# Kernel tuning notes

Measured on AMD Instinct MI355X. Metric: run time of the kernel, lower is better.

## Reference

```python
import jax, jax.numpy as jnp
import numpy as np

D_MODEL = 1024
NUM_HEADS = 16

def setup_inputs() -> dict:
    key = jax.random.key(0)
    ks = jax.random.split(key, 9)
    d = D_MODEL
    s = 0.02
    return {
        "x": jax.random.normal(ks[0], (2, 2048, d), dtype=jnp.float32),
        "wq": jax.random.normal(ks[1], (d, d), dtype=jnp.float32) * s,
        "bq": jax.random.normal(ks[2], (d,), dtype=jnp.float32) * s,
        "wk": jax.random.normal(ks[3], (d, d), dtype=jnp.float32) * s,
        "bk": jax.random.normal(ks[4], (d,), dtype=jnp.float32) * s,
        "wv": jax.random.normal(ks[5], (d, d), dtype=jnp.float32) * s,
        "bv": jax.random.normal(ks[6], (d,), dtype=jnp.float32) * s,
        "wo": jax.random.normal(ks[7], (d, d), dtype=jnp.float32) * s,
        "bo": jax.random.normal(ks[8], (d,), dtype=jnp.float32) * s,
    }

def reference(x, wq, bq, wk, bk, wv, bv, wo, bo) -> jnp.ndarray:
    b, s, d = x.shape
    h = NUM_HEADS
    dk = d // h
    # projections (torch Linear: x @ W^T + b)
    q = x @ wq.T + bq
    k = x @ wk.T + bk
    v = x @ wv.T + bv
    # split heads -> [b, h, s, dk]
    q = q.reshape(b, s, h, dk).transpose(0, 2, 1, 3)
    k = k.reshape(b, s, h, dk).transpose(0, 2, 1, 3)
    v = v.reshape(b, s, h, dk).transpose(0, 2, 1, 3)
    scale = jnp.sqrt(jnp.asarray(dk, dtype=x.dtype))
    scores = jnp.einsum('bhqd,bhkd->bhqk', q, k) / scale
    causal = jnp.tril(jnp.ones((s, s), dtype=bool))  # [s, s]
    scores = jnp.where(causal[None, None], scores, jnp.asarray(-jnp.inf, dtype=x.dtype))
    attn = jax.nn.softmax(scores, axis=-1)
    out = jnp.einsum('bhqk,bhkd->bhqd', attn, v)
    out = out.transpose(0, 2, 1, 3).reshape(b, s, d)
    return out @ wo.T + bo
```

## Files before the change

### kernel.cpp

```cpp
#include <hip/hip_runtime.h>

#define D_MODEL 1024
#define NHEAD   16
#define DK      64
#define BATCH   2
#define SEQ     2048
#define M_TOT   (BATCH*SEQ)

typedef unsigned short u16;
typedef unsigned int   u32;
typedef __attribute__((ext_vector_type(8))) __bf16 bf16x8;
typedef __attribute__((ext_vector_type(8))) u16   u16x8;
typedef __attribute__((ext_vector_type(4))) u16   u16x4;
typedef __attribute__((ext_vector_type(4))) float f32x4;

typedef const __attribute__((address_space(1))) u32* gas_ptr;
typedef __attribute__((address_space(3))) u32*       las_ptr;

__device__ __forceinline__ void gload16(const u16* g, u16* l) {
  __builtin_amdgcn_global_load_lds((gas_ptr)g, (las_ptr)l, 16, 0, 0);
}

__device__ __forceinline__ u16 bfc(float f) {
  union { __bf16 h; u16 u; } v; v.h = (__bf16)f; return v.u;
}

__global__ void cvt_all(const float* __restrict__ x,
                        const float* __restrict__ wq, const float* __restrict__ wk,
                        const float* __restrict__ wv, const float* __restrict__ wo,
                        u16* __restrict__ xbf, u16* __restrict__ wbf) {
  const int y = blockIdx.y;
  const float* src;
  u16* dst;
  int n8;
  if (y == 0)      { src = x;  dst = xbf;                n8 = M_TOT * D_MODEL / 8; }
  else if (y == 1) { src = wq; dst = wbf;                n8 = 1024 * 1024 / 8; }
  else if (y == 2) { src = wk; dst = wbf + 1 * 1048576;  n8 = 1024 * 1024 / 8; }
  else if (y == 3) { src = wv; dst = wbf + 2 * 1048576;  n8 = 1024 * 1024 / 8; }
  else             { src = wo; dst = wbf + 3 * 1048576;  n8 = 1024 * 1024 / 8; }
  for (int i = blockIdx.x * blockDim.x + threadIdx.x; i < n8; i += gridDim.x * blockDim.x) {
    const float4* s = (const float4*)src + (size_t)i * 2;
    float4 a = s[0], b = s[1];
    u16x8 o;
    o[0]=bfc(a.x); o[1]=bfc(a.y); o[2]=bfc(a.z); o[3]=bfc(a.w);
    o[4]=bfc(b.x); o[5]=bfc(b.y); o[6]=bfc(b.z); o[7]=bfc(b.w);
    *((u16x8*)dst + i) = o;
  }
}

#define QSCALE 0.18033688011112042f

__global__ __launch_bounds__(256) void qkv_gemm(
    const u16* __restrict__ xbf, const u16* __restrict__ wbf,
    const float* __restrict__ bq, const float* __restrict__ bk, const float* __restrict__ bv,
    u16* __restrict__ qws, u16* __restrict__ kws, u16* __restrict__ vtws)
{
  __shared__ u16 la[2 * 128 * 32];
  __shared__ u16 lb[2 * 64 * 32];
  const int z     = blockIdx.z;
  const int nbase = blockIdx.x * 64;
  const int mbase = blockIdx.y * 128;
  const u16*  A    = xbf;
  const u16*  Bm   = wbf + (size_t)z * 1024 * 1024;
  const float* bias = (z == 0) ? bq : (z == 1) ? bk : bv;

  const int tid  = threadIdx.x;
  const int lane = tid & 63;
  const int wid  = tid >> 6;
  const int wr   = (wid >> 1) * 64, wc = (wid & 1) * 32;
  const int lr   = lane & 15, lg = lane >> 4;
  const int srow = tid >> 2;
  const int sc   = tid & 3;
  const int sdst = srow * 32 + sc * 8;
  const int ssrc = (sc ^ ((srow >> 1) & 3)) * 8;
  const int csw  = (lg ^ ((lr >> 1) & 3)) * 8;

  f32x4 acc[4][2];
  #pragma unroll
  for (int i = 0; i < 4; ++i) { acc[i][0] = (f32x4){0,0,0,0}; acc[i][1] = (f32x4){0,0,0,0}; }

  {
    gload16(&A [(size_t)(mbase + srow)      * 1024 + ssrc], &la[sdst]);
    gload16(&A [(size_t)(mbase + srow + 64) * 1024 + ssrc], &la[64*32 + sdst]);
    gload16(&Bm[(size_t)(nbase + srow)      * 1024 + ssrc], &lb[sdst]);
  }
  __syncthreads();
  int cur = 0;
  for (int k0 = 0; k0 < 1024; k0 += 32) {
    if (k0 + 32 < 1024) {
      const int nb = cur ^ 1;
      gload16(&A [(size_t)(mbase + srow)      * 1024 + k0 + 32 + ssrc], &la[nb*4096 + sdst]);
      gload16(&A [(size_t)(mbase + srow + 64) * 1024 + k0 + 32 + ssrc], &la[nb*4096 + 64*32 + sdst]);
      gload16(&Bm[(size_t)(nbase + srow)      * 1024 + k0 + 32 + ssrc], &lb[nb*2048 + sdst]);
    }
    bf16x8 af[4], bfr[2];
    #pragma unroll
    for (int i = 0; i < 4; ++i)
      af[i] = *(const bf16x8*)&la[cur*4096 + (wr + i*16 + lr)*32 + csw];
    #pragma unroll
    for (int j = 0; j < 2; ++j)
      bfr[j] = *(const bf16x8*)&lb[cur*2048 + (wc + j*16 + lr)*32 + csw];
    #pragma unroll
    for (int i = 0; i < 4; ++i)
      #pragma unroll
      for (int j = 0; j < 2; ++j)
        acc[i][j] = __builtin_amdgcn_mfma_f32_16x16x32_bf16(af[i], bfr[j], acc[i][j], 0, 0, 0);
    __syncthreads();
    cur ^= 1;
  }

  #pragma unroll
  for (int i = 0; i < 4; ++i) {
    #pragma unroll
    for (int j = 0; j < 2; ++j) {
      int gn = nbase + wc + j*16 + lr;
      float bs = bias[gn];
      int h = gn >> 6, d = gn & 63;
      int gm0 = mbase + wr + i*16 + lg*4;
      int bb = gm0 >> 11, s0 = gm0 & 2047;
      if (z == 2) {
        u16x4 vk;
        #pragma unroll
        for (int r = 0; r < 4; ++r) vk[r] = bfc(acc[i][j][r] + bs);
        *(u16x4*)&vtws[(((size_t)(bb*NHEAD + h)) * DK + d) * SEQ + s0] = vk;
      } else {
        #pragma unroll
        for (int r = 0; r < 4; ++r) {
          float v = acc[i][j][r] + bs;
          if (z == 0) qws[(((size_t)(bb*NHEAD + h)) * SEQ + s0 + r) * DK + d] = bfc(v * QSCALE);
          else        kws[(((size_t)(bb*NHEAD + h)) * SEQ + s0 + r) * DK + d] = bfc(v);
        }
      }
    }
  }
}

__global__ __launch_bounds__(256) void out_gemm(
    const u16* __restrict__ ows, const u16* __restrict__ wobf,
    const float* __restrict__ bo, float* __restrict__ out)
{
  __shared__ u16 la[2 * 64 * 64];
  __shared__ u16 lb[2 * 64 * 64];
  const int nbase = blockIdx.x * 64;
  const int mbase = blockIdx.y * 64;
  const int tid  = threadIdx.x;
  const int lane = tid & 63;
  const int wid  = tid >> 6;
  const int wr   = (wid >> 1) * 32, wc = (wid & 1) * 32;
  const int lr   = lane & 15, lg = lane >> 4;
  const int srow = tid >> 3;
  const int sc   = tid & 7;
  const int sdst = srow * 64 + sc * 8;
  const int ssrc = (sc ^ (srow & 7)) * 8;
  const int lsw  = lr & 7;

  f32x4 acc[2][2];
  acc[0][0] = (f32x4){0,0,0,0}; acc[0][1] = (f32x4){0,0,0,0};
  acc[1][0] = (f32x4){0,0,0,0}; acc[1][1] = (f32x4){0,0,0,0};

  {
    gload16(&ows [(size_t)(mbase + srow)      * 1024 + ssrc], &la[sdst]);
    gload16(&ows [(size_t)(mbase + srow + 32) * 1024 + ssrc], &la[32*64 + sdst]);
    gload16(&wobf[(size_t)(nbase + srow)      * 1024 + ssrc], &lb[sdst]);
    gload16(&wobf[(size_t)(nbase + srow + 32) * 1024 + ssrc], &lb[32*64 + sdst]);
  }
  __syncthreads();
  int cur = 0;
  for (int k0 = 0; k0 < 1024; k0 += 64) {
    if (k0 + 64 < 1024) {
      const int nb = cur ^ 1;
      gload16(&ows [(size_t)(mbase + srow)      * 1024 + k0 + 64 + ssrc], &la[nb*4096 + sdst]);
      gload16(&ows [(size_t)(mbase + srow + 32) * 1024 + k0 + 64 + ssrc], &la[nb*4096 + 32*64 + sdst]);
      gload16(&wobf[(size_t)(nbase + srow)      * 1024 + k0 + 64 + ssrc], &lb[nb*4096 + sdst]);
      gload16(&wobf[(size_t)(nbase + srow + 32) * 1024 + k0 + 64 + ssrc], &lb[nb*4096 + 32*64 + sdst]);
    }
    bf16x8 af[2][2], bfr[2][2];
    #pragma unroll
    for (int kk = 0; kk < 2; ++kk) {
      #pragma unroll
      for (int i = 0; i < 2; ++i)
        af[i][kk] = *(const bf16x8*)&la[cur*4096 + (wr + i*16 + lr)*64 + (((kk*4 + lg) ^ lsw) * 8)];
      #pragma unroll
      for (int j = 0; j < 2; ++j)
        bfr[j][kk] = *(const bf16x8*)&lb[cur*4096 + (wc + j*16 + lr)*64 + (((kk*4 + lg) ^ lsw) * 8)];
    }
    #pragma unroll
    for (int kk = 0; kk < 2; ++kk)
      #pragma unroll
      for (int i = 0; i < 2; ++i)
        #pragma unroll
        for (int j = 0; j < 2; ++j)
          acc[i][j] = __builtin_amdgcn_mfma_f32_16x16x32_bf16(af[i][kk], bfr[j][kk], acc[i][j], 0, 0, 0);
    __syncthreads();
    cur ^= 1;
  }

  #pragma unroll
  for (int i = 0; i < 2; ++i) {
    #pragma unroll
    for (int j = 0; j < 2; ++j) {
      int gn = nbase + wc + j*16 + lr;
      float bs = bo[gn];
      #pragma unroll
      for (int r = 0; r < 4; ++r) {
        int gm = mbase + wr + i*16 + lg*4 + r;
        out[(size_t)gm * 1024 + gn] = acc[i][j][r] + bs;
      }
    }
  }
}

__global__ __launch_bounds__(256) void attn_kernel(
    const u16* __restrict__ qws, const u16* __restrict__ kws,
    const u16* __restrict__ vtws, u16* __restrict__ ows)
{
  __shared__ u16 kbuf[2 * 64 * 64];
  __shared__ u16 vbuf[2 * 64 * 64];
  __shared__ u16 pbuf[4 * 16 * 64];
  const int flat = blockIdx.x;
  const int r    = flat & 7;
  const int g    = flat >> 3;
  const int bh_l = g >> 5;
  const int qp   = g & 31;
  const int qt   = (bh_l & 1) ? qp : (31 - qp);
  const int bh   = r * 4 + bh_l;
  const int b = bh >> 4, h = bh & 15;
  const int tid = threadIdx.x, wid = tid >> 6, lane = tid & 63;
  const int lr = lane & 15, lg = lane >> 4;
  const u16* Q  = qws  + (size_t)(b * NHEAD + h) * SEQ * DK;
  const u16* K  = kws  + (size_t)(b * NHEAD + h) * SEQ * DK;
  const u16* Vt = vtws + (size_t)(b * NHEAD + h) * DK * SEQ;

  const int sr  = tid >> 3;
  const int sc8 = (tid & 7) * 8;
  const int c0s = ((tid & 7) ^ (sr & 7)) * 8;
  const int c1s = ((tid & 7) ^ ((sr + 32) & 7)) * 8;

  #define STAGE(u, bi) do { \
    const int kb_ = (u) * 64; \
    const int off_ = (bi) * 4096; \
    gload16(&K[(size_t)(kb_ + sr) * DK + c0s],        &kbuf[off_ + sr * 64 + sc8]); \
    gload16(&K[(size_t)(kb_ + sr + 32) * DK + c1s],   &kbuf[off_ + (sr + 32) * 64 + sc8]); \
    gload16(&Vt[(size_t)sr * SEQ + kb_ + c0s],        &vbuf[off_ + sr * 64 + sc8]); \
    gload16(&Vt[(size_t)(sr + 32) * SEQ + kb_ + c1s], &vbuf[off_ + (sr + 32) * 64 + sc8]); \
  } while (0)
  #define CH(m) ((((m)*4 + lg) ^ (lr & 7)) * 8)

  const int qbase  = qt * 64 + wid * 16;
  const int q_glob = qbase + lr;

  bf16x8 qf0 = *(const bf16x8*)&Q[(size_t)q_glob * DK + lg * 8];
  bf16x8 qf1 = *(const bf16x8*)&Q[(size_t)q_glob * DK + 32 + lg * 8];

  f32x4 oacc[4];
  #pragma unroll
  for (int t = 0; t < 4; ++t) oacc[t] = (f32x4){0.f, 0.f, 0.f, 0.f};
  float l_run = 0.f;

  STAGE(0, 0);
  __syncthreads();

  int cur = 0;
  for (int t = 0; t <= qt; ++t) {
    if (t < qt) STAGE(t + 1, cur ^ 1);

    const int diag = (t == qt);
    const int nsub = diag ? (wid + 1) : 4;
    const int cb = cur * 4096;

    f32x4 sacc[4];
    __builtin_amdgcn_s_setprio(1);
    #pragma unroll
    for (int ts = 0; ts < 4; ++ts) {
      if (ts >= nsub) continue;
      bf16x8 kf0 = *(const bf16x8*)&kbuf[cb + (ts*16 + lr) * 64 + CH(0)];
      bf16x8 kf1 = *(const bf16x8*)&kbuf[cb + (ts*16 + lr) * 64 + CH(1)];
      f32x4 s0 = (f32x4){0.f, 0.f, 0.f, 0.f};
      s0 = __builtin_amdgcn_mfma_f32_16x16x32_bf16(kf0, qf0, s0, 0, 0, 0);
      s0 = __builtin_amdgcn_mfma_f32_16x16x32_bf16(kf1, qf1, s0, 0, 0, 0);
      sacc[ts] = s0;
    }
    __builtin_amdgcn_s_setprio(0);
    if (diag) {
      const int ts = wid;
      #pragma unroll
      for (int r2 = 0; r2 < 4; ++r2)
        if (lg * 4 + r2 > lr) sacc[ts][r2] = -1e30f;
    }
    #pragma unroll
    for (int ts = 0; ts < 4; ++ts) {
      if (ts >= nsub) continue;
      #pragma unroll
      for (int r2 = 0; r2 < 4; ++r2) {
        float p = __builtin_amdgcn_exp2f(sacc[ts][r2]);
        sacc[ts][r2] = p;
        l_run += p;
      }
    }

    #pragma unroll
    for (int ts = 0; ts < 4; ++ts) {
      u16x4 pk;
      if (ts < nsub) {
        pk[0] = bfc(sacc[ts][0]); pk[1] = bfc(sacc[ts][1]);
        pk[2] = bfc(sacc[ts][2]); pk[3] = bfc(sacc[ts][3]);
      } else {
        pk[0] = 0; pk[1] = 0; pk[2] = 0; pk[3] = 0;
      }
      const int pc = (((ts*2 + (lg >> 1)) ^ (lr & 7)) * 8) + (lg & 1) * 4;
      *(u16x4*)&pbuf[wid * 1024 + lr * 64 + pc] = pk;
    }
    asm volatile("s_waitcnt lgkmcnt(0)" ::: "memory");
    __builtin_amdgcn_sched_barrier(0);
    bf16x8 pf0 = *(const bf16x8*)&pbuf[wid * 1024 + lr * 64 + CH(0)];
    bf16x8 pf1 = *(const bf16x8*)&pbuf[wid * 1024 + lr * 64 + CH(1)];

    __builtin_amdgcn_s_setprio(1);
    #pragma unroll
    for (int td = 0; td < 4; ++td) {
      bf16x8 vf0 = *(const bf16x8*)&vbuf[cb + (td*16 + lr) * 64 + CH(0)];
      bf16x8 vf1 = *(const bf16x8*)&vbuf[cb + (td*16 + lr) * 64 + CH(1)];
      oacc[td] = __builtin_amdgcn_mfma_f32_16x16x32_bf16(vf0, pf0, oacc[td], 0, 0, 0);
      oacc[td] = __builtin_amdgcn_mfma_f32_16x16x32_bf16(vf1, pf1, oacc[td], 0, 0, 0);
    }
    __builtin_amdgcn_s_setprio(0);
    __syncthreads();
    cur ^= 1;
  }

  float l_tot = l_run;
  l_tot += __shfl_xor(l_tot, 16);
  l_tot += __shfl_xor(l_tot, 32);
  const float inv = 1.0f / l_tot;
  #pragma unroll
  for (int td = 0; td < 4; ++td) {
    u16x4 ok;
    #pragma unroll
    for (int r2 = 0; r2 < 4; ++r2) ok[r2] = bfc(oacc[td][r2] * inv);
    *(u16x4*)&ows[((size_t)(b * SEQ + q_glob)) * D_MODEL + h * DK + td*16 + lg*4] = ok;
  }
  #undef CH
  #undef STAGE
}

extern "C" void kernel_launch(void* const* d_in, const int* in_sizes, int n_in,
                              void* d_out, int out_size, void* d_ws, size_t ws_size,
                              hipStream_t stream) {
  const float* x  = (const float*)d_in[0];
  const float* wq = (const float*)d_in[1];
  const float* bq = (const float*)d_in[2];
  const float* wk = (const float*)d_in[3];
  const float* bk = (const float*)d_in[4];
  const float* wv = (const float*)d_in[5];
  const float* bv = (const float*)d_in[6];
  const float* wo = (const float*)d_in[7];
  const float* bo = (const float*)d_in[8];
  float* out = (float*)d_out;

  char* ws = (char*)d_ws;
  u16* qws  = (u16*)(ws + (size_t) 0 * (1 << 20));
  u16* kws  = (u16*)(ws + (size_t) 8 * (1 << 20));
  u16* vtws = (u16*)(ws + (size_t)16 * (1 << 20));
  u16* ows  = (u16*)(ws + (size_t)24 * (1 << 20));
  u16* xbf  = (u16*)(ws + (size_t)32 * (1 << 20));
  u16* wbf  = (u16*)(ws + (size_t)40 * (1 << 20));

  cvt_all<<<dim3(512, 5), 256, 0, stream>>>(x, wq, wk, wv, wo, xbf, wbf);

  qkv_gemm<<<dim3(1024 / 64, M_TOT / 128, 3), 256, 0, stream>>>(
      xbf, wbf, bq, bk, bv, qws, kws, vtws);

  attn_kernel<<<dim3(1024, 1, 1), 256, 0, stream>>>(qws, kws, vtws, ows);

  out_gemm<<<dim3(1024 / 64, M_TOT / 64), 256, 0, stream>>>(
      ows, wbf + (size_t)3 * 1024 * 1024, bo, out);
}
```

Measured before the change: 111.6 us.

## Prefetch two stages ahead with explicit vmcnt waits in GEMMs and attention

Replaces the simple double-buffer loops in the QKV projection, output projection and attention kernels with a two-deep prefetch. Two tiles are issued up front, each iteration waits with a partial s_waitcnt vmcnt so only the oldest tile's loads must have landed, and raw s_barrier calls fenced by sched_barrier replace __syncthreads. This keeps more global-to-LDS loads in flight so memory latency overlaps with MFMA work. The hand-counted vmcnt values must match the number of loads issued per stage, or the code reads stale data.

```diff
diff --git a/kernel.cpp b/kernel.cpp
--- a/kernel.cpp
+++ b/kernel.cpp
@@ -24,6 +24,12 @@
 __device__ __forceinline__ u16 bfc(float f) {
   union { __bf16 h; u16 u; } v; v.h = (__bf16)f; return v.u;
 }
+
+#define BAR() do { \
+  __builtin_amdgcn_sched_barrier(0); \
+  __builtin_amdgcn_s_barrier(); \
+  __builtin_amdgcn_sched_barrier(0); \
+} while (0)
 
 __global__ void cvt_all(const float* __restrict__ x,
                         const float* __restrict__ wq, const float* __restrict__ wk,
@@ -79,35 +85,36 @@
   #pragma unroll
   for (int i = 0; i < 4; ++i) { acc[i][0] = (f32x4){0,0,0,0}; acc[i][1] = (f32x4){0,0,0,0}; }
 
-  {
-    gload16(&A [(size_t)(mbase + srow)      * 1024 + ssrc], &la[sdst]);
-    gload16(&A [(size_t)(mbase + srow + 64) * 1024 + ssrc], &la[64*32 + sdst]);
-    gload16(&Bm[(size_t)(nbase + srow)      * 1024 + ssrc], &lb[sdst]);
-  }
-  __syncthreads();
-  int cur = 0;
-  for (int k0 = 0; k0 < 1024; k0 += 32) {
-    if (k0 + 32 < 1024) {
-      const int nb = cur ^ 1;
-      gload16(&A [(size_t)(mbase + srow)      * 1024 + k0 + 32 + ssrc], &la[nb*4096 + sdst]);
-      gload16(&A [(size_t)(mbase + srow + 64) * 1024 + k0 + 32 + ssrc], &la[nb*4096 + 64*32 + sdst]);
-      gload16(&Bm[(size_t)(nbase + srow)      * 1024 + k0 + 32 + ssrc], &lb[nb*2048 + sdst]);
-    }
+  #define STAGEQ(u, bi) do { \
+    const int k0_ = (u) * 32; \
+    gload16(&A [(size_t)(mbase + srow)      * 1024 + k0_ + ssrc], &la[(bi)*4096 + sdst]); \
+    gload16(&A [(size_t)(mbase + srow + 64) * 1024 + k0_ + ssrc], &la[(bi)*4096 + 64*32 + sdst]); \
+    gload16(&Bm[(size_t)(nbase + srow)      * 1024 + k0_ + ssrc], &lb[(bi)*2048 + sdst]); \
+  } while (0)
+
+  STAGEQ(0, 0);
+  STAGEQ(1, 1);
+  for (int t = 0; t < 32; ++t) {
+    if (t < 31) asm volatile("s_waitcnt vmcnt(3)" ::: "memory");
+    else        asm volatile("s_waitcnt vmcnt(0)" ::: "memory");
+    BAR();
+    const int cb = (t & 1) * 4096, cbb = (t & 1) * 2048;
     bf16x8 af[4], bfr[2];
     #pragma unroll
     for (int i = 0; i < 4; ++i)
-      af[i] = *(const bf16x8*)&la[cur*4096 + (wr + i*16 + lr)*32 + csw];
+      af[i] = *(const bf16x8*)&la[cb + (wr + i*16 + lr)*32 + csw];
     #pragma unroll
     for (int j = 0; j < 2; ++j)
-      bfr[j] = *(const bf16x8*)&lb[cur*2048 + (wc + j*16 + lr)*32 + csw];
+      bfr[j] = *(const bf16x8*)&lb[cbb + (wc + j*16 + lr)*32 + csw];
     #pragma unroll
     for (int i = 0; i < 4; ++i)
       #pragma unroll
       for (int j = 0; j < 2; ++j)
         acc[i][j] = __builtin_amdgcn_mfma_f32_16x16x32_bf16(af[i], bfr[j], acc[i][j], 0, 0, 0);
-    __syncthreads();
-    cur ^= 1;
-  }
+    BAR();
+    if (t + 2 < 32) STAGEQ(t + 2, t & 1);
+  }
+  #undef STAGEQ
 
   #pragma unroll
   for (int i = 0; i < 4; ++i) {
@@ -158,31 +165,30 @@
   acc[0][0] = (f32x4){0,0,0,0}; acc[0][1] = (f32x4){0,0,0,0};
   acc[1][0] = (f32x4){0,0,0,0}; acc[1][1] = (f32x4){0,0,0,0};
 
-  {
-    gload16(&ows [(size_t)(mbase + srow)      * 1024 + ssrc], &la[sdst]);
-    gload16(&ows [(size_t)(mbase + srow + 32) * 1024 + ssrc], &la[32*64 + sdst]);
-    gload16(&wobf[(size_t)(nbase + srow)      * 1024 + ssrc], &lb[sdst]);
-    gload16(&wobf[(size_t)(nbase + srow + 32) * 1024 + ssrc], &lb[32*64 + sdst]);
-  }
-  __syncthreads();
-  int cur = 0;
-  for (int k0 = 0; k0 < 1024; k0 += 64) {
-    if (k0 + 64 < 1024) {
-      const int nb = cur ^ 1;
-      gload16(&ows [(size_t)(mbase + srow)      * 1024 + k0 + 64 + ssrc], &la[nb*4096 + sdst]);
-      gload16(&ows [(size_t)(mbase + srow + 32) * 1024 + k0 + 64 + ssrc], &la[nb*4096 + 32*64 + sdst]);
-      gload16(&wobf[(size_t)(nbase + srow)      * 1024 + k0 + 64 + ssrc], &lb[nb*4096 + sdst]);
-      gload16(&wobf[(size_t)(nbase + srow + 32) * 1024 + k0 + 64 + ssrc], &lb[nb*4096 + 32*64 + sdst]);
-    }
+  #define STAGEO(u, bi) do { \
+    const int k0_ = (u) * 64; \
+    gload16(&ows [(size_t)(mbase + srow)      * 1024 + k0_ + ssrc], &la[(bi)*4096 + sdst]); \
+    gload16(&ows [(size_t)(mbase + srow + 32) * 1024 + k0_ + ssrc], &la[(bi)*4096 + 32*64 + sdst]); \
+    gload16(&wobf[(size_t)(nbase + srow)      * 1024 + k0_ + ssrc], &lb[(bi)*4096 + sdst]); \
+    gload16(&wobf[(size_t)(nbase + srow + 32) * 1024 + k0_ + ssrc], &lb[(bi)*4096 + 32*64 + sdst]); \
+  } while (0)
+
+  STAGEO(0, 0);
+  STAGEO(1, 1);
+  for (int t = 0; t < 16; ++t) {
+    if (t < 15) asm volatile("s_waitcnt vmcnt(4)" ::: "memory");
+    else        asm volatile("s_waitcnt vmcnt(0)" ::: "memory");
+    BAR();
+    const int cb = (t & 1) * 4096;
     bf16x8 af[2][2], bfr[2][2];
     #pragma unroll
     for (int kk = 0; kk < 2; ++kk) {
       #pragma unroll
       for (int i = 0; i < 2; ++i)
-        af[i][kk] = *(const bf16x8*)&la[cur*4096 + (wr + i*16 + lr)*64 + (((kk*4 + lg) ^ lsw) * 8)];
+        af[i][kk] = *(const bf16x8*)&la[cb + (wr + i*16 + lr)*64 + (((kk*4 + lg) ^ lsw) * 8)];
       #pragma unroll
       for (int j = 0; j < 2; ++j)
-        bfr[j][kk] = *(const bf16x8*)&lb[cur*4096 + (wc + j*16 + lr)*64 + (((kk*4 + lg) ^ lsw) * 8)];
+        bfr[j][kk] = *(const bf16x8*)&lb[cb + (wc + j*16 + lr)*64 + (((kk*4 + lg) ^ lsw) * 8)];
     }
     #pragma unroll
     for (int kk = 0; kk < 2; ++kk)
@@ -191,9 +197,10 @@
         #pragma unroll
         for (int j = 0; j < 2; ++j)
           acc[i][j] = __builtin_amdgcn_mfma_f32_16x16x32_bf16(af[i][kk], bfr[j][kk], acc[i][j], 0, 0, 0);
-    __syncthreads();
-    cur ^= 1;
-  }
+    BAR();
+    if (t + 2 < 16) STAGEO(t + 2, t & 1);
+  }
+  #undef STAGEO
 
   #pragma unroll
   for (int i = 0; i < 2; ++i) {
@@ -258,15 +265,16 @@
   float l_run = 0.f;
 
   STAGE(0, 0);
-  __syncthreads();
-
-  int cur = 0;
+  if (qt >= 1) STAGE(1, 1);
+
   for (int t = 0; t <= qt; ++t) {
-    if (t < qt) STAGE(t + 1, cur ^ 1);
+    if (t < qt) asm volatile("s_waitcnt vmcnt(4)" ::: "memory");
+    else        asm volatile("s_waitcnt vmcnt(0)" ::: "memory");
+    BAR();
 
     const int diag = (t == qt);
     const int nsub = diag ? (wid + 1) : 4;
-    const int cb = cur * 4096;
+    const int cb = (t & 1) * 4096;
 
     f32x4 sacc[4];
     __builtin_amdgcn_s_setprio(1);
@@ -324,8 +332,8 @@
       oacc[td] = __builtin_amdgcn_mfma_f32_16x16x32_bf16(vf1, pf1, oacc[td], 0, 0, 0);
     }
     __builtin_amdgcn_s_setprio(0);
-    __syncthreads();
-    cur ^= 1;
+    BAR();
+    if (t + 2 <= qt) STAGE(t + 2, t & 1);
   }
 
   float l_tot = l_run;
```

Result: no change. 113.4 us (+1.6%).

## Remap GEMM blocks per XCD and prefetch attention K/V two tiles ahead

Applied to the files above, without the earlier changes.

The QKV and output GEMMs now use a flattened 1D grid. Block indices are remapped so that blocks landing on the same XCD share the same M rows, which should improve L2 reuse of the activation tiles. The attention loop now issues K/V loads two tiles ahead and waits with vmcnt-based partial waits plus raw s_barrier, instead of staging one tile ahead under __syncthreads. This hides more global-load latency but depends on an exact count of outstanding loads per stage, so a miscount could break correctness.

```diff
diff --git a/kernel.cpp b/kernel.cpp
--- a/kernel.cpp
+++ b/kernel.cpp
@@ -24,6 +24,12 @@
 __device__ __forceinline__ u16 bfc(float f) {
   union { __bf16 h; u16 u; } v; v.h = (__bf16)f; return v.u;
 }
+
+#define BAR() do { \
+  __builtin_amdgcn_sched_barrier(0); \
+  __builtin_amdgcn_s_barrier(); \
+  __builtin_amdgcn_sched_barrier(0); \
+} while (0)
 
 __global__ void cvt_all(const float* __restrict__ x,
                         const float* __restrict__ wq, const float* __restrict__ wk,
@@ -57,9 +63,13 @@
 {
   __shared__ u16 la[2 * 128 * 32];
   __shared__ u16 lb[2 * 64 * 32];
-  const int z     = blockIdx.z;
-  const int nbase = blockIdx.x * 64;
-  const int mbase = blockIdx.y * 128;
+  const int flat = blockIdx.x;
+  const int xcd  = flat & 7;
+  const int loc  = flat >> 3;
+  const int z    = loc >> 6;
+  const int rem  = loc & 63;
+  const int nbase = (rem & 15) * 64;
+  const int mbase = (xcd * 4 + (rem >> 4)) * 128;
   const u16*  A    = xbf;
   const u16*  Bm   = wbf + (size_t)z * 1024 * 1024;
   const float* bias = (z == 0) ? bq : (z == 1) ? bk : bv;
@@ -141,8 +151,11 @@
 {
   __shared__ u16 la[2 * 64 * 64];
   __shared__ u16 lb[2 * 64 * 64];
-  const int nbase = blockIdx.x * 64;
-  const int mbase = blockIdx.y * 64;
+  const int flat = blockIdx.x;
+  const int xcd  = flat & 7;
+  const int loc  = flat >> 3;
+  const int nbase = (loc & 15) * 64;
+  const int mbase = (xcd * 8 + (loc >> 4)) * 64;
   const int tid  = threadIdx.x;
   const int lane = tid & 63;
   const int wid  = tid >> 6;
@@ -258,15 +271,16 @@
   float l_run = 0.f;
 
   STAGE(0, 0);
-  __syncthreads();
-
-  int cur = 0;
+  if (qt >= 1) STAGE(1, 1);
+
   for (int t = 0; t <= qt; ++t) {
-    if (t < qt) STAGE(t + 1, cur ^ 1);
+    if (t < qt) asm volatile("s_waitcnt vmcnt(4)" ::: "memory");
+    else        asm volatile("s_waitcnt vmcnt(0)" ::: "memory");
+    BAR();
 
     const int diag = (t == qt);
     const int nsub = diag ? (wid + 1) : 4;
-    const int cb = cur * 4096;
+    const int cb = (t & 1) * 4096;
 
     f32x4 sacc[4];
     __builtin_amdgcn_s_setprio(1);
@@ -324,8 +338,8 @@
       oacc[td] = __builtin_amdgcn_mfma_f32_16x16x32_bf16(vf1, pf1, oacc[td], 0, 0, 0);
     }
     __builtin_amdgcn_s_setprio(0);
-    __syncthreads();
-    cur ^= 1;
+    BAR();
+    if (t + 2 <= qt) STAGE(t + 2, t & 1);
   }
 
   float l_tot = l_run;
@@ -367,11 +381,11 @@
 
   cvt_all<<<dim3(512, 5), 256, 0, stream>>>(x, wq, wk, wv, wo, xbf, wbf);
 
-  qkv_gemm<<<dim3(1024 / 64, M_TOT / 128, 3), 256, 0, stream>>>(
+  qkv_gemm<<<dim3(1536, 1, 1), 256, 0, stream>>>(
       xbf, wbf, bq, bk, bv, qws, kws, vtws);
 
   attn_kernel<<<dim3(1024, 1, 1), 256, 0, stream>>>(qws, kws, vtws, ows);
 
-  out_gemm<<<dim3(1024 / 64, M_TOT / 64), 256, 0, stream>>>(
+  out_gemm<<<dim3(1024, 1, 1), 256, 0, stream>>>(
       ows, wbf + (size_t)3 * 1024 * 1024, bo, out);
 }
```

New measurement: 108.6 us, median of 3. -2.7%, faster.
